# Optimization experiments

Measured on AMD Instinct MI355X. Metric: run time of the kernel, lower is better.

## Reference

```python
import jax, jax.numpy as jnp
import numpy as np

N_NODES = 50000
N_EDGES = 800000
D_IN, D_HID, D_OUT = 128, 128, 256
EPS = 1e-12  # F.normalize eps


def _mean_aggr(h, src, dst, n):
    # scatter-mean of source features onto destination nodes
    msg_sum = jax.ops.segment_sum(h[src], dst, num_segments=n)
    deg = jax.ops.segment_sum(jnp.ones((src.shape[0],), h.dtype), dst, num_segments=n)
    return msg_sum / jnp.maximum(deg, 1.0)[:, None]


def _l2_normalize(h):
    # F.normalize(p=2, dim=1): divide by clamped L2 norm
    nrm = jnp.sqrt(jnp.sum(h * h, axis=1, keepdims=True))
    return h / jnp.maximum(nrm, EPS)


def setup_inputs() -> dict:
    key = jax.random.key(0)
    ks = jax.random.split(key, 8)
    x = jax.random.normal(ks[0], (N_NODES, D_IN), dtype=jnp.float32)
    edge_index = jax.random.randint(ks[1], (2, N_EDGES), 0, N_NODES, dtype=jnp.int64 if jax.config.read('jax_enable_x64') else jnp.int32)
    s = 1.0 / np.sqrt(D_IN)
    W1_l = jax.random.uniform(ks[2], (D_IN, D_HID), jnp.float32, -s, s)
    W1_r = jax.random.uniform(ks[3], (D_IN, D_HID), jnp.float32, -s, s)
    b1 = jnp.zeros((D_HID,), jnp.float32)
    s2 = 1.0 / np.sqrt(D_HID)
    W2_l = jax.random.uniform(ks[4], (D_HID, D_OUT), jnp.float32, -s2, s2)
    W2_r = jax.random.uniform(ks[5], (D_HID, D_OUT), jnp.float32, -s2, s2)
    b2 = jnp.zeros((D_OUT,), jnp.float32)
    return {"x": x, "edge_index": edge_index, "W1_l": W1_l, "W1_r": W1_r,
            "b1": b1, "W2_l": W2_l, "W2_r": W2_r, "b2": b2}


def reference(x, edge_index, W1_l, W1_r, b1, W2_l, W2_r, b2):
    src, dst = edge_index[0], edge_index[1]
    n = x.shape[0]
    # SAGEConv 1: lin_l(mean_aggr(x)) + lin_r(x) + bias
    h = _mean_aggr(x, src, dst, n) @ W1_l + x @ W1_r + b1
    # dropout is identity in eval mode
    h = _l2_normalize(jax.nn.sigmoid(h))
    # SAGEConv 2
    h = _mean_aggr(h, src, dst, n) @ W2_l + h @ W2_r + b2
    h = _l2_normalize(jax.nn.sigmoid(h))
    return jax.nn.log_softmax(h, axis=-1)
```

## Files before the change

### kernel.cpp

```cpp
#include <hip/hip_runtime.h>

#define NN 50000
#define NE 800000
#define NB 782
#define CAP 1536


__device__ __forceinline__ unsigned short f2bf(float f) {
    union { float f; unsigned u; } v; v.f = f;
    unsigned u = v.u;
    return (unsigned short)((u + 0x7fffu + ((u >> 16) & 1u)) >> 16);
}
__device__ __forceinline__ float bfu_lo(unsigned p) {
    union { unsigned u; float f; } v; v.u = p << 16; return v.f;
}
__device__ __forceinline__ float bfu_hi(unsigned p) {
    union { unsigned u; float f; } v; v.u = p & 0xffff0000u; return v.f;
}

typedef __bf16 bf16x8 __attribute__((ext_vector_type(8)));
typedef float f32x4 __attribute__((ext_vector_type(4)));
union U16 { uint4 u; bf16x8 v; };


__global__ __launch_bounds__(512) void binscatter_kernel(const int* __restrict__ src,
                                                         const int* __restrict__ dst,
                                                         int* __restrict__ bcnt,
                                                         unsigned* __restrict__ ebuf) {
    __shared__ int hist[NB];
    __shared__ int base[NB];
    const int BE = 8192;
    int tid = threadIdx.x;
    int e0 = blockIdx.x * BE;
    for (int i = tid; i < NB; i += 512) hist[i] = 0;
    __syncthreads();
    for (int i = tid; i < BE; i += 512) {
        int e = e0 + i;
        if (e < NE) atomicAdd(&hist[dst[e] >> 6], 1);
    }
    __syncthreads();
    for (int i = tid; i < NB; i += 512) {
        int c = hist[i];
        base[i] = c ? atomicAdd(&bcnt[i], c) : 0;
        hist[i] = 0;
    }
    __syncthreads();
    for (int i = tid; i < BE; i += 512) {
        int e = e0 + i;
        if (e < NE) {
            int d = dst[e], b = d >> 6;
            int slot = base[b] + atomicAdd(&hist[b], 1);
            if (slot < CAP)
                ebuf[(size_t)b * CAP + slot] = (unsigned)src[e] | ((unsigned)(d & 63) << 16);
        }
    }
}

__global__ __launch_bounds__(256) void csr_kernel(const int* __restrict__ bcnt,
                                                  const unsigned* __restrict__ ebuf,
                                                  int* __restrict__ rowptr,
                                                  int* __restrict__ col) {
    __shared__ int red[256];
    __shared__ int deg[64];
    __shared__ int cur[64];
    __shared__ int cbase_s;
    int b = blockIdx.x, tid = threadIdx.x;
    int s = 0;
    for (int i = tid; i < b; i += 256) s += bcnt[i];
    red[tid] = s;
    if (tid < 64) deg[tid] = 0;
    __syncthreads();
    for (int off = 128; off; off >>= 1) {
        if (tid < off) red[tid] += red[tid + off];
        __syncthreads();
    }
    if (tid == 0) cbase_s = red[0];
    __syncthreads();
    int cnt = bcnt[b], cbase = cbase_s;
    if (cnt > CAP) cnt = CAP;
    const unsigned* eb = ebuf + (size_t)b * CAP;
    for (int i = tid; i < cnt; i += 256) atomicAdd(&deg[(eb[i] >> 16) & 63], 1);
    __syncthreads();
    if (tid == 0) {
        int run = 0;
        for (int j = 0; j < 64; j++) { cur[j] = run; run += deg[j]; }
    }
    __syncthreads();
    int node = b * 64 + tid;
    if (tid < 64 && node < NN) rowptr[node] = cbase + cur[tid];
    if (b == NB - 1 && tid == 0) rowptr[NN] = NE;
    __syncthreads();
    for (int i = tid; i < cnt; i += 256) {
        unsigned e = eb[i];
        int pos = atomicAdd(&cur[(e >> 16) & 63], 1);
        col[cbase + pos] = (int)(e & 0xffffu);
    }
}


template <int N>
__device__ __forceinline__ void pack_one(const float* __restrict__ Wl,
                                         const float* __restrict__ Wr,
                                         unsigned short* __restrict__ Wp, int t) {
    int lane = t & 63, c = t >> 6;
    int ks = c & 7, nt = c >> 3;
    int n = nt * 16 + (lane & 15);
    int kq = ks * 32 + (lane >> 4) * 8;
    unsigned short tmp[8];
#pragma unroll
    for (int j = 0; j < 8; j++) {
        int k = kq + j;
        float w = (k < 128) ? Wl[(size_t)k * N + n] : Wr[(size_t)(k - 128) * N + n];
        tmp[j] = f2bf(w);
    }
    ((ushort4*)Wp)[(size_t)c * 128 + lane * 2 + 0] = make_ushort4(tmp[0], tmp[1], tmp[2], tmp[3]);
    ((ushort4*)Wp)[(size_t)c * 128 + lane * 2 + 1] = make_ushort4(tmp[4], tmp[5], tmp[6], tmp[7]);
}

#define CAST_BLK (NN * 128 / 4 / 256)

__global__ void castpack_kernel(const float* __restrict__ in, unsigned short* __restrict__ outp,
                                const float* __restrict__ W1l, const float* __restrict__ W1r,
                                unsigned short* __restrict__ W1p,
                                const float* __restrict__ W2l, const float* __restrict__ W2r,
                                unsigned short* __restrict__ W2p) {
    if (blockIdx.x < CAST_BLK) {
        int i = blockIdx.x * 256 + threadIdx.x;
        float4 f = ((const float4*)in)[i];
        ushort4 o;
        o.x = f2bf(f.x); o.y = f2bf(f.y); o.z = f2bf(f.z); o.w = f2bf(f.w);
        ((ushort4*)outp)[i] = o;
    } else {
        int t = (blockIdx.x - CAST_BLK) * 256 + threadIdx.x;
        if (t < 8 * 8 * 64) pack_one<128>(W1l, W1r, W1p, t);
        else if (t < 8 * 8 * 64 + 16 * 8 * 64) pack_one<256>(W2l, W2r, W2p, t - 8 * 8 * 64);
    }
}


__global__ void aggregate_bf_kernel(const int* __restrict__ rowptr, const int* __restrict__ col,
                                    const uint4* __restrict__ feat4,
                                    uint4* __restrict__ out4) {
    int wid = (blockIdx.x * blockDim.x + threadIdx.x) >> 6;
    int lane = threadIdx.x & 63;
    if (wid >= NN) return;
    int beg = rowptr[wid], end = rowptr[wid + 1];
    int deg = end - beg;
    int g = lane >> 4, c16 = lane & 15;
    int nmain = deg < 64 ? deg : 64;
    int cidx = (lane < nmain) ? col[beg + lane] : 0;
    float acc[8];
#pragma unroll
    for (int j = 0; j < 8; j++) acc[j] = 0.f;
    for (int i = 0; i < nmain; i += 8) {
        int e0 = i + g, e1 = i + 4 + g;
        int s0 = __shfl(cidx, e0);
        int s1 = __shfl(cidx, e1);
        uint4 v0 = make_uint4(0u, 0u, 0u, 0u);
        uint4 v1 = make_uint4(0u, 0u, 0u, 0u);
        if (e0 < nmain) v0 = feat4[(size_t)s0 * 16 + c16];
        if (e1 < nmain) v1 = feat4[(size_t)s1 * 16 + c16];
        acc[0] += bfu_lo(v0.x); acc[1] += bfu_hi(v0.x);
        acc[2] += bfu_lo(v0.y); acc[3] += bfu_hi(v0.y);
        acc[4] += bfu_lo(v0.z); acc[5] += bfu_hi(v0.z);
        acc[6] += bfu_lo(v0.w); acc[7] += bfu_hi(v0.w);
        acc[0] += bfu_lo(v1.x); acc[1] += bfu_hi(v1.x);
        acc[2] += bfu_lo(v1.y); acc[3] += bfu_hi(v1.y);
        acc[4] += bfu_lo(v1.z); acc[5] += bfu_hi(v1.z);
        acc[6] += bfu_lo(v1.w); acc[7] += bfu_hi(v1.w);
    }
    for (int i = 64; i < deg; i += 4) {
        int idx = beg + i + g;
        if (idx < end) {
            int s = col[idx];
            uint4 v = feat4[(size_t)s * 16 + c16];
            acc[0] += bfu_lo(v.x); acc[1] += bfu_hi(v.x);
            acc[2] += bfu_lo(v.y); acc[3] += bfu_hi(v.y);
            acc[4] += bfu_lo(v.z); acc[5] += bfu_hi(v.z);
            acc[6] += bfu_lo(v.w); acc[7] += bfu_hi(v.w);
        }
    }
#pragma unroll
    for (int j = 0; j < 8; j++) {
        acc[j] += __shfl_xor(acc[j], 16);
        acc[j] += __shfl_xor(acc[j], 32);
    }
    if (g == 0) {
        float inv = (deg > 0) ? 1.0f / (float)deg : 0.0f;
        uint4 o;
        o.x = (unsigned)f2bf(acc[0] * inv) | ((unsigned)f2bf(acc[1] * inv) << 16);
        o.y = (unsigned)f2bf(acc[2] * inv) | ((unsigned)f2bf(acc[3] * inv) << 16);
        o.z = (unsigned)f2bf(acc[4] * inv) | ((unsigned)f2bf(acc[5] * inv) << 16);
        o.w = (unsigned)f2bf(acc[6] * inv) | ((unsigned)f2bf(acc[7] * inv) << 16);
        out4[(size_t)wid * 16 + c16] = o;
    }
}


template <int N, bool FINAL>
__global__ __launch_bounds__(256) void gemm_mfma_kernel(
    const unsigned short* __restrict__ A0, const unsigned short* __restrict__ A1,
    const unsigned short* __restrict__ Wp, const float* __restrict__ bias,
    void* __restrict__ outp, int M) {
    const int NT = N / 16;
    int tid = threadIdx.x, wave = tid >> 6, lane = tid & 63;
    int quad = lane >> 4, col = lane & 15;
    int m_base = blockIdx.x * 64 + wave * 16;
    int row = m_base + col;
    int row_ld = row < M ? row : M - 1;

    bf16x8 a[8];
    const uint4* a0p = (const uint4*)(A0 + (size_t)row_ld * 128 + quad * 8);
    const uint4* a1p = (const uint4*)(A1 + (size_t)row_ld * 128 + quad * 8);
#pragma unroll
    for (int ks = 0; ks < 4; ks++) { U16 u; u.u = a0p[ks * 4]; a[ks] = u.v; }
#pragma unroll
    for (int ks = 0; ks < 4; ks++) { U16 u; u.u = a1p[ks * 4]; a[4 + ks] = u.v; }

    f32x4 acc[NT];
#pragma unroll
    for (int nt = 0; nt < NT; nt++) acc[nt] = (f32x4){0.f, 0.f, 0.f, 0.f};

    const uint4* wp = (const uint4*)Wp;
#pragma unroll
    for (int nt = 0; nt < NT; nt++) {
#pragma unroll
        for (int ks = 0; ks < 8; ks++) {
            U16 u; u.u = wp[(size_t)(nt * 8 + ks) * 64 + lane];
            acc[nt] = __builtin_amdgcn_mfma_f32_16x16x32_bf16(a[ks], u.v, acc[nt], 0, 0, 0);
        }
    }

    float ssq[4] = {0.f, 0.f, 0.f, 0.f};
#pragma unroll
    for (int nt = 0; nt < NT; nt++) {
        float bv = bias[nt * 16 + col];
#pragma unroll
        for (int r = 0; r < 4; r++) {
            float z = acc[nt][r] + bv;
            float s = 1.0f / (1.0f + __expf(-z));
            acc[nt][r] = s;
            ssq[r] += s * s;
        }
    }
#pragma unroll
    for (int r = 0; r < 4; r++) {
#pragma unroll
        for (int off = 1; off < 16; off <<= 1) ssq[r] += __shfl_xor(ssq[r], off, 16);
        float sc = 1.0f / fmaxf(sqrtf(ssq[r]), 1e-12f);
#pragma unroll
        for (int nt = 0; nt < NT; nt++) acc[nt][r] *= sc;
    }

    if (FINAL) {
#pragma unroll
        for (int r = 0; r < 4; r++) {
            float mx = -1e30f;
#pragma unroll
            for (int nt = 0; nt < NT; nt++) mx = fmaxf(mx, acc[nt][r]);
#pragma unroll
            for (int off = 1; off < 16; off <<= 1) mx = fmaxf(mx, __shfl_xor(mx, off, 16));
            float se = 0.f;
#pragma unroll
            for (int nt = 0; nt < NT; nt++) se += __expf(acc[nt][r] - mx);
#pragma unroll
            for (int off = 1; off < 16; off <<= 1) se += __shfl_xor(se, off, 16);
            float lse = mx + __logf(se);
#pragma unroll
            for (int nt = 0; nt < NT; nt++) acc[nt][r] -= lse;
        }
        float* op = (float*)outp;
#pragma unroll
        for (int r = 0; r < 4; r++) {
            int m = m_base + quad * 4 + r;
            if (m < M) {
#pragma unroll
                for (int nt = 0; nt < NT; nt++) op[(size_t)m * N + nt * 16 + col] = acc[nt][r];
            }
        }
    } else {
        unsigned short* op = (unsigned short*)outp;
#pragma unroll
        for (int r = 0; r < 4; r++) {
            int m = m_base + quad * 4 + r;
            if (m < M) {
#pragma unroll
                for (int nt = 0; nt < NT; nt++)
                    op[(size_t)m * N + nt * 16 + col] = f2bf(acc[nt][r]);
            }
        }
    }
}


extern "C" void kernel_launch(void* const* d_in, const int* in_sizes, int n_in,
                              void* d_out, int out_size, void* d_ws, size_t ws_size,
                              hipStream_t stream) {
    const float* x   = (const float*)d_in[0];
    const int*   ei  = (const int*)d_in[1];
    const float* W1l = (const float*)d_in[2];
    const float* W1r = (const float*)d_in[3];
    const float* b1  = (const float*)d_in[4];
    const float* W2l = (const float*)d_in[5];
    const float* W2r = (const float*)d_in[6];
    const float* b2  = (const float*)d_in[7];
    float* out = (float*)d_out;

    const int* src = ei;
    const int* dst = ei + NE;

    char* ws = (char*)d_ws;
    size_t off = 0;
    auto alloc = [&](size_t bytes) -> void* {
        void* p = ws + off;
        off += (bytes + 255) / 256 * 256;
        return p;
    };
    int* rowptr     = (int*)alloc((size_t)(NN + 1) * 4);
    int* col        = (int*)alloc((size_t)NE * 4);
    int* bcnt       = (int*)alloc((size_t)NB * 4);
    unsigned* ebuf  = (unsigned*)alloc((size_t)NB * CAP * 4);
    unsigned short* x_bf   = (unsigned short*)alloc((size_t)NN * 128 * 2);
    unsigned short* agg_bf = (unsigned short*)alloc((size_t)NN * 128 * 2);
    unsigned short* h1_bf  = (unsigned short*)alloc((size_t)NN * 128 * 2);
    unsigned short* W1p    = (unsigned short*)alloc((size_t)8 * 8 * 64 * 8 * 2);
    unsigned short* W2p    = (unsigned short*)alloc((size_t)16 * 8 * 64 * 8 * 2);

    hipMemsetAsync(bcnt, 0, (size_t)NB * 4, stream);
    binscatter_kernel<<<(NE + 8191) / 8192, 512, 0, stream>>>(src, dst, bcnt, ebuf);
    csr_kernel<<<NB, 256, 0, stream>>>(bcnt, ebuf, rowptr, col);

    castpack_kernel<<<CAST_BLK + 48, 256, 0, stream>>>(x, x_bf, W1l, W1r, W1p, W2l, W2r, W2p);

    aggregate_bf_kernel<<<(NN + 3) / 4, 256, 0, stream>>>(rowptr, col, (const uint4*)x_bf,
                                                          (uint4*)agg_bf);
    gemm_mfma_kernel<128, false><<<(NN + 63) / 64, 256, 0, stream>>>(agg_bf, x_bf, W1p, b1,
                                                                     h1_bf, NN);
    aggregate_bf_kernel<<<(NN + 3) / 4, 256, 0, stream>>>(rowptr, col, (const uint4*)h1_bf,
                                                          (uint4*)agg_bf);
    gemm_mfma_kernel<256, true><<<(NN + 63) / 64, 256, 0, stream>>>(agg_bf, h1_bf, W2p, b2,
                                                                    out, NN);
}
```

Baseline: 235.5 us.

## Stage packed weights in LDS and use persistent grid-stride GEMM blocks

The GEMM kernels now copy the packed weight matrix into shared memory once per block using global_load_lds and run a persistent grid of 256 blocks of 512 threads. Each wave walks 16-row tiles in a grid-stride loop, so weights are no longer re-read from global/L2 for every 16-row tile. The final softmax also drops the max subtraction, since values after L2 normalization lie in [0,1]. The changes add large LDS use (up to 128KB for N=256), which can limit occupancy, and a fixed grid size that may underfill the device.

```diff
diff --git a/kernel.cpp b/kernel.cpp
--- a/kernel.cpp
+++ b/kernel.cpp
@@ -21,6 +21,12 @@
 typedef __bf16 bf16x8 __attribute__((ext_vector_type(8)));
 typedef float f32x4 __attribute__((ext_vector_type(4)));
 union U16 { uint4 u; bf16x8 v; };
+
+typedef unsigned int u32_as1 __attribute__((address_space(1)));
+typedef unsigned int u32_as3 __attribute__((address_space(3)));
+__device__ __forceinline__ void gload_lds16(const void* g, void* l) {
+    __builtin_amdgcn_global_load_lds((const u32_as1*)g, (u32_as3*)l, 16, 0, 0);
+}
 
 
 __global__ __launch_bounds__(512) void binscatter_kernel(const int* __restrict__ src,
@@ -198,95 +204,108 @@
 
 
 template <int N, bool FINAL>
-__global__ __launch_bounds__(256) void gemm_mfma_kernel(
+__global__ __launch_bounds__(512, 2) void gemm_mfma_kernel(
     const unsigned short* __restrict__ A0, const unsigned short* __restrict__ A1,
     const unsigned short* __restrict__ Wp, const float* __restrict__ bias,
     void* __restrict__ outp, int M) {
     const int NT = N / 16;
+    __shared__ unsigned char sW[NT * 8192];
     int tid = threadIdx.x, wave = tid >> 6, lane = tid & 63;
     int quad = lane >> 4, col = lane & 15;
-    int m_base = blockIdx.x * 64 + wave * 16;
-    int row = m_base + col;
-    int row_ld = row < M ? row : M - 1;
-
-    bf16x8 a[8];
-    const uint4* a0p = (const uint4*)(A0 + (size_t)row_ld * 128 + quad * 8);
-    const uint4* a1p = (const uint4*)(A1 + (size_t)row_ld * 128 + quad * 8);
-#pragma unroll
-    for (int ks = 0; ks < 4; ks++) { U16 u; u.u = a0p[ks * 4]; a[ks] = u.v; }
-#pragma unroll
-    for (int ks = 0; ks < 4; ks++) { U16 u; u.u = a1p[ks * 4]; a[4 + ks] = u.v; }
-
-    f32x4 acc[NT];
-#pragma unroll
-    for (int nt = 0; nt < NT; nt++) acc[nt] = (f32x4){0.f, 0.f, 0.f, 0.f};
-
-    const uint4* wp = (const uint4*)Wp;
-#pragma unroll
-    for (int nt = 0; nt < NT; nt++) {
+
+    {
+        const char* gs = (const char*)Wp + wave * (NT * 1024);
+        char* ld = (char*)sW + wave * (NT * 1024);
+#pragma unroll
+        for (int j = 0; j < NT; j++) gload_lds16(gs + j * 1024 + lane * 16, ld + j * 1024);
+    }
+
+    float bv[NT];
+#pragma unroll
+    for (int nt = 0; nt < NT; nt++) bv[nt] = bias[nt * 16 + col];
+
+    __syncthreads();
+
+    const int T = (M + 15) >> 4;
+    const int wstride = gridDim.x << 3;
+    for (int t = blockIdx.x * 8 + wave; t < T; t += wstride) {
+        int m_base = t * 16;
+        int row = m_base + col;
+        int row_ld = row < M ? row : M - 1;
+
+        bf16x8 a[8];
+        const uint4* a0p = (const uint4*)(A0 + (size_t)row_ld * 128 + quad * 8);
+        const uint4* a1p = (const uint4*)(A1 + (size_t)row_ld * 128 + quad * 8);
+#pragma unroll
+        for (int ks = 0; ks < 4; ks++) { U16 u; u.u = a0p[ks * 4]; a[ks] = u.v; }
+#pragma unroll
+        for (int ks = 0; ks < 4; ks++) { U16 u; u.u = a1p[ks * 4]; a[4 + ks] = u.v; }
+
+        f32x4 acc[NT];
+#pragma unroll
+        for (int nt = 0; nt < NT; nt++) acc[nt] = (f32x4){0.f, 0.f, 0.f, 0.f};
+
 #pragma unroll
         for (int ks = 0; ks < 8; ks++) {
-            U16 u; u.u = wp[(size_t)(nt * 8 + ks) * 64 + lane];
-            acc[nt] = __builtin_amdgcn_mfma_f32_16x16x32_bf16(a[ks], u.v, acc[nt], 0, 0, 0);
-        }
-    }
-
-    float ssq[4] = {0.f, 0.f, 0.f, 0.f};
-#pragma unroll
-    for (int nt = 0; nt < NT; nt++) {
-        float bv = bias[nt * 16 + col];
+#pragma unroll
+            for (int nt = 0; nt < NT; nt++) {
+                U16 u; u.u = *(const uint4*)(sW + (nt * 8 + ks) * 1024 + lane * 16);
+                acc[nt] = __builtin_amdgcn_mfma_f32_16x16x32_bf16(a[ks], u.v, acc[nt], 0, 0, 0);
+            }
+        }
+
+        float ssq[4] = {0.f, 0.f, 0.f, 0.f};
+#pragma unroll
+        for (int nt = 0; nt < NT; nt++) {
+#pragma unroll
+            for (int r = 0; r < 4; r++) {
+                float z = acc[nt][r] + bv[nt];
+                float s = 1.0f / (1.0f + __expf(-z));
+                acc[nt][r] = s;
+                ssq[r] += s * s;
+            }
+        }
 #pragma unroll
         for (int r = 0; r < 4; r++) {
-            float z = acc[nt][r] + bv;
-            float s = 1.0f / (1.0f + __expf(-z));
-            acc[nt][r] = s;
-            ssq[r] += s * s;
-        }
-    }
-#pragma unroll
-    for (int r = 0; r < 4; r++) {
-#pragma unroll
-        for (int off = 1; off < 16; off <<= 1) ssq[r] += __shfl_xor(ssq[r], off, 16);
-        float sc = 1.0f / fmaxf(sqrtf(ssq[r]), 1e-12f);
-#pragma unroll
-        for (int nt = 0; nt < NT; nt++) acc[nt][r] *= sc;
-    }
-
-    if (FINAL) {
-#pragma unroll
-        for (int r = 0; r < 4; r++) {
-            float mx = -1e30f;
-#pragma unroll
-            for (int nt = 0; nt < NT; nt++) mx = fmaxf(mx, acc[nt][r]);
-#pragma unroll
-            for (int off = 1; off < 16; off <<= 1) mx = fmaxf(mx, __shfl_xor(mx, off, 16));
-            float se = 0.f;
-#pragma unroll
-            for (int nt = 0; nt < NT; nt++) se += __expf(acc[nt][r] - mx);
-#pragma unroll
-            for (int off = 1; off < 16; off <<= 1) se += __shfl_xor(se, off, 16);
-            float lse = mx + __logf(se);
-#pragma unroll
-            for (int nt = 0; nt < NT; nt++) acc[nt][r] -= lse;
-        }
-        float* op = (float*)outp;
-#pragma unroll
-        for (int r = 0; r < 4; r++) {
-            int m = m_base + quad * 4 + r;
-            if (m < M) {
-#pragma unroll
-                for (int nt = 0; nt < NT; nt++) op[(size_t)m * N + nt * 16 + col] = acc[nt][r];
-            }
-        }
-    } else {
-        unsigned short* op = (unsigned short*)outp;
-#pragma unroll
-        for (int r = 0; r < 4; r++) {
-            int m = m_base + quad * 4 + r;
-            if (m < M) {
-#pragma unroll
-                for (int nt = 0; nt < NT; nt++)
-                    op[(size_t)m * N + nt * 16 + col] = f2bf(acc[nt][r]);
+#pragma unroll
+            for (int off = 1; off < 16; off <<= 1) ssq[r] += __shfl_xor(ssq[r], off, 16);
+            float sc = 1.0f / fmaxf(sqrtf(ssq[r]), 1e-12f);
+#pragma unroll
+            for (int nt = 0; nt < NT; nt++) acc[nt][r] *= sc;
+        }
+
+        if (FINAL) {
+#pragma unroll
+            for (int r = 0; r < 4; r++) {
+                float se = 0.f;
+#pragma unroll
+                for (int nt = 0; nt < NT; nt++) se += __expf(acc[nt][r]);
+#pragma unroll
+                for (int off = 1; off < 16; off <<= 1) se += __shfl_xor(se, off, 16);
+                float lse = __logf(se);
+#pragma unroll
+                for (int nt = 0; nt < NT; nt++) acc[nt][r] -= lse;
+            }
+            float* op = (float*)outp;
+#pragma unroll
+            for (int r = 0; r < 4; r++) {
+                int m = m_base + quad * 4 + r;
+                if (m < M) {
+#pragma unroll
+                    for (int nt = 0; nt < NT; nt++)
+                        op[(size_t)m * N + nt * 16 + col] = acc[nt][r];
+                }
+            }
+        } else {
+            unsigned short* op = (unsigned short*)outp;
+#pragma unroll
+            for (int r = 0; r < 4; r++) {
+                int m = m_base + quad * 4 + r;
+                if (m < M) {
+#pragma unroll
+                    for (int nt = 0; nt < NT; nt++)
+                        op[(size_t)m * N + nt * 16 + col] = f2bf(acc[nt][r]);
+                }
             }
         }
     }
@@ -334,10 +353,8 @@
 
     aggregate_bf_kernel<<<(NN + 3) / 4, 256, 0, stream>>>(rowptr, col, (const uint4*)x_bf,
                                                           (uint4*)agg_bf);
-    gemm_mfma_kernel<128, false><<<(NN + 63) / 64, 256, 0, stream>>>(agg_bf, x_bf, W1p, b1,
-                                                                     h1_bf, NN);
+    gemm_mfma_kernel<128, false><<<256, 512, 0, stream>>>(agg_bf, x_bf, W1p, b1, h1_bf, NN);
     aggregate_bf_kernel<<<(NN + 3) / 4, 256, 0, stream>>>(rowptr, col, (const uint4*)h1_bf,
                                                           (uint4*)agg_bf);
-    gemm_mfma_kernel<256, true><<<(NN + 63) / 64, 256, 0, stream>>>(agg_bf, h1_bf, W2p, b2,
-                                                                    out, NN);
-}
+    gemm_mfma_kernel<256, true><<<256, 512, 0, stream>>>(agg_bf, h1_bf, W2p, b2, out, NN);
+}
```

New measurement: 392.2 us. +66.5%, slower.
